# Optimization experiments

Measured on AMD Instinct MI355X. Metric: run time of the kernel, lower is better.

Reference implementation:

```python
import jax, jax.numpy as jnp
import numpy as np

B, C, K, G = 512, 1000, 8, 8   # batch, num classes, boxes per image, grid size
IMG_SIZE = 256.0
L1, L2, L3 = 1.0, 5.0, 1.0     # loss weights (init_kwargs)
LOG_CLAMP = -100.0             # torch BCE clamps log to -100


def setup_inputs() -> dict:
    key = jax.random.key(0)
    k1, k2, k3, k4, k5 = jax.random.split(key, 5)
    # channel 0 is post-sigmoid objectness, so uniform [0,1) is valid for BCE
    outputs = jax.random.uniform(k1, (B, 5 + C, G, G), dtype=jnp.float32)
    boxes = jax.random.uniform(k2, (B, K, 4), dtype=jnp.float32) * IMG_SIZE  # pixel coords
    labels = jax.random.randint(k3, (B, K), 1, C + 1, dtype=jnp.int32)       # 1..C
    box_xy = jax.random.randint(k4, (B, K, 2), 0, G, dtype=jnp.int32)        # (x, y) grid cells
    obj_target = jax.random.uniform(k5, (B, G * G), dtype=jnp.float32)
    return dict(outputs=outputs, boxes=boxes, labels=labels, box_xy=box_xy,
                obj_target=obj_target)


def reference(outputs, boxes, labels, box_xy, obj_target):
    b = outputs.shape[0]

    # ---- objectness BCE (mean over B*64) ----
    p = outputs[:, 0].reshape(b, G * G)
    logp = jnp.maximum(jnp.log(p), LOG_CLAMP)
    log1mp = jnp.maximum(jnp.log1p(-p), LOG_CLAMP)
    cel_obj = -(obj_target * logp + (1.0 - obj_target) * log1mp).mean()

    # ---- gather per-box values at grid cells ----
    bi = jnp.arange(b)[:, None]          # (B,1) broadcasts with (B,K)
    x = box_xy[..., 0]                   # (B,K)
    y = box_xy[..., 1]                   # (B,K)

    # class CE: logits at each box cell, shape (B,K,C)
    cls_logits = outputs[:, 5:][bi, :, y, x]
    ce = jax.nn.logsumexp(cls_logits, axis=-1) - jnp.take_along_axis(
        cls_logits, (labels - 1)[..., None].astype(jnp.int32), axis=-1)[..., 0]
    cel_class = ce.sum() / b             # sum over all boxes, / batch_size

    # bbox MSE: original detaches predictions via .item(), so stop_gradient
    p_box = jax.lax.stop_gradient(outputs[:, 1:5][bi, :, y, x])  # (B,K,4)
    target = jnp.round(boxes / IMG_SIZE * 10.0) / 10.0           # np.round(x/IMG, 1)
    bb_loss = ((p_box - target) ** 2).mean(axis=-1).sum() / b

    total = L1 * cel_obj + L2 * bb_loss + L3 * cel_class
    return total, cel_obj, bb_loss, cel_class
```

## Files before the change

### kernel.cpp

```cpp
#include <hip/hip_runtime.h>
#include <math.h>

#define NB   512
#define NC   1000
#define NK   8
#define PL   64
#define NCH  1005

__global__ __launch_bounds__(512, 4) void yolo_main(
    const float* __restrict__ out,
    const float* __restrict__ boxes,
    const int*   __restrict__ labels,
    const int*   __restrict__ box_xy,
    const float* __restrict__ obj_t,
    float* __restrict__ ws)
{
    const int b    = blockIdx.x;
    const int tid  = threadIdx.x;
    const int w    = tid >> 6;
    const int lane = tid & 63;

    const float*  img = out + (size_t)b * (NCH * PL);
    const float4* p4  = (const float4*)(img + 5 * PL);

    float s0 = 0.f, s1 = 0.f, s2 = 0.f, s3 = 0.f;

    float4 buf[8];
    #pragma unroll
    for (int j = 0; j < 8; ++j) buf[j] = p4[j * 512 + tid];

    #pragma unroll
    for (int t = 0; t < 31; ++t) {
        const float4 v = buf[t & 7];
        if (t < 23) buf[t & 7] = p4[(t + 8) * 512 + tid];
        s0 += __expf(v.x);
        s1 += __expf(v.y);
        s2 += __expf(v.z);
        s3 += __expf(v.w);
    }
    if (tid < 128) {
        const float4 v = p4[15872 + tid];
        s0 += __expf(v.x);
        s1 += __expf(v.y);
        s2 += __expf(v.z);
        s3 += __expf(v.w);
    }

    __shared__ float sm_s[32][64];
    __shared__ float lse_sh[64];
    {
        const int pid = tid >> 4;
        const int q   = tid & 15;
        ((float4*)sm_s[pid])[q] = make_float4(s0, s1, s2, s3);
    }
    __syncthreads();

    float obj_v = 0.f, ce_v = 0.f, bb_v = 0.f;

    if (w == 0) {
        float S = 0.f;
        #pragma unroll
        for (int i = 0; i < 32; ++i) S += sm_s[i][lane];
        lse_sh[lane] = __logf(S);

        const float p   = img[lane];
        const float tt  = obj_t[b * PL + lane];
        const float lp  = fmaxf(__logf(p),  -100.0f);
        const float l1p = fmaxf(log1pf(-p), -100.0f);
        obj_v = -(tt * lp + (1.0f - tt) * l1p);
    }
    __syncthreads();

    if (w == 0 && lane < NK) {
        const int k    = lane;
        const int x    = box_xy[(b * NK + k) * 2 + 0];
        const int y    = box_xy[(b * NK + k) * 2 + 1];
        const int cell = y * 8 + x;
        const int lab  = labels[b * NK + k] - 1;

        const float logit = img[(size_t)(5 + lab) * PL + cell];
        ce_v = lse_sh[cell] - logit;

        float acc = 0.f;
        #pragma unroll
        for (int j = 0; j < 4; ++j) {
            const float pb = img[(size_t)(1 + j) * PL + cell];
            const float tv = rintf(boxes[(b * NK + k) * 4 + j] * (10.0f / 256.0f)) / 10.0f;
            const float d  = pb - tv;
            acc += d * d;
        }
        bb_v = 0.25f * acc;
    }

    if (w == 0) {
        #pragma unroll
        for (int off = 32; off > 0; off >>= 1) {
            obj_v += __shfl_down(obj_v, off);
            ce_v  += __shfl_down(ce_v,  off);
            bb_v  += __shfl_down(bb_v,  off);
        }
        if (lane == 0) {
            ws[b]          = obj_v;
            ws[NB + b]     = ce_v;
            ws[2 * NB + b] = bb_v;
        }
    }
}

__global__ __launch_bounds__(512) void yolo_finish(
    const float* __restrict__ ws, float* __restrict__ dout)
{
    __shared__ float r0[NB], r1[NB], r2[NB];
    const int tid = threadIdx.x;
    r0[tid] = ws[tid];
    r1[tid] = ws[NB + tid];
    r2[tid] = ws[2 * NB + tid];
    __syncthreads();
    for (int off = 256; off > 0; off >>= 1) {
        if (tid < off) {
            r0[tid] += r0[tid + off];
            r1[tid] += r1[tid + off];
            r2[tid] += r2[tid + off];
        }
        __syncthreads();
    }
    if (tid == 0) {
        const float cel_obj   = r0[0] / 32768.0f;
        const float cel_class = r1[0] / 512.0f;
        const float bb_loss   = r2[0] / 512.0f;
        dout[0] = cel_obj + 5.0f * bb_loss + cel_class;
        dout[1] = cel_obj;
        dout[2] = bb_loss;
        dout[3] = cel_class;
    }
}

extern "C" void kernel_launch(void* const* d_in, const int* in_sizes, int n_in,
                              void* d_out, int out_size, void* d_ws, size_t ws_size,
                              hipStream_t stream) {
    const float* outputs = (const float*)d_in[0];
    const float* boxes   = (const float*)d_in[1];
    const int*   labels  = (const int*)d_in[2];
    const int*   box_xy  = (const int*)d_in[3];
    const float* obj_t   = (const float*)d_in[4];
    float* ws   = (float*)d_ws;
    float* dout = (float*)d_out;

    yolo_main<<<NB, 512, 0, stream>>>(outputs, boxes, labels, box_xy, obj_t, ws);
    yolo_finish<<<1, 512, 0, stream>>>(ws, dout);
}
```

Before: 27.67 us.

## Fuse final reduction via last-block atomic counter and hoist gathers before LSE

Merges the separate finish kernel into the main kernel: each block bumps a global counter and the last block to finish reduces the per-block partials and writes the outputs. The scalar gathers (objectness BCE, box MSE, label logit) are also moved ahead of the streaming exp-sum so their latency overlaps with it, which removes one __syncthreads. This trades a second kernel launch for a memset launch plus an atomic and fence per block.

```diff
diff --git a/kernel.cpp b/kernel.cpp
--- a/kernel.cpp
+++ b/kernel.cpp
@@ -7,13 +7,15 @@
 #define PL   64
 #define NCH  1005
 
-__global__ __launch_bounds__(512, 4) void yolo_main(
+__global__ __launch_bounds__(512, 4) void yolo_fused(
     const float* __restrict__ out,
     const float* __restrict__ boxes,
     const int*   __restrict__ labels,
     const int*   __restrict__ box_xy,
     const float* __restrict__ obj_t,
-    float* __restrict__ ws)
+    float* __restrict__ ws,
+    int*   __restrict__ counter,
+    float* __restrict__ dout)
 {
     const int b    = blockIdx.x;
     const int tid  = threadIdx.x;
@@ -23,8 +25,36 @@
     const float*  img = out + (size_t)b * (NCH * PL);
     const float4* p4  = (const float4*)(img + 5 * PL);
 
+    float obj_v = 0.f, ce_v = 0.f, bb_v = 0.f, logit = 0.f;
+    int cell = 0;
+    if (w == 0) {
+        const float p   = img[lane];
+        const float tt  = obj_t[b * PL + lane];
+        const float lp  = fmaxf(__logf(p),  -100.0f);
+        const float l1p = fmaxf(log1pf(-p), -100.0f);
+        obj_v = -(tt * lp + (1.0f - tt) * l1p);
+
+        if (lane < NK) {
+            const int k   = lane;
+            const int x   = box_xy[(b * NK + k) * 2 + 0];
+            const int y   = box_xy[(b * NK + k) * 2 + 1];
+            cell          = y * 8 + x;
+            const int lab = labels[b * NK + k] - 1;
+            logit = img[(size_t)(5 + lab) * PL + cell];
+
+            float acc = 0.f;
+            #pragma unroll
+            for (int j = 0; j < 4; ++j) {
+                const float pb = img[(size_t)(1 + j) * PL + cell];
+                const float tv = rintf(boxes[(b * NK + k) * 4 + j] * (10.0f / 256.0f)) / 10.0f;
+                const float d  = pb - tv;
+                acc += d * d;
+            }
+            bb_v = 0.25f * acc;
+        }
+    }
+
     float s0 = 0.f, s1 = 0.f, s2 = 0.f, s3 = 0.f;
-
     float4 buf[8];
     #pragma unroll
     for (int j = 0; j < 8; ++j) buf[j] = p4[j * 512 + tid];
@@ -55,44 +85,13 @@
     }
     __syncthreads();
 
-    float obj_v = 0.f, ce_v = 0.f, bb_v = 0.f;
-
     if (w == 0) {
         float S = 0.f;
         #pragma unroll
         for (int i = 0; i < 32; ++i) S += sm_s[i][lane];
         lse_sh[lane] = __logf(S);
+        ce_v = (lane < NK) ? (lse_sh[cell] - logit) : 0.f;
 
-        const float p   = img[lane];
-        const float tt  = obj_t[b * PL + lane];
-        const float lp  = fmaxf(__logf(p),  -100.0f);
-        const float l1p = fmaxf(log1pf(-p), -100.0f);
-        obj_v = -(tt * lp + (1.0f - tt) * l1p);
-    }
-    __syncthreads();
-
-    if (w == 0 && lane < NK) {
-        const int k    = lane;
-        const int x    = box_xy[(b * NK + k) * 2 + 0];
-        const int y    = box_xy[(b * NK + k) * 2 + 1];
-        const int cell = y * 8 + x;
-        const int lab  = labels[b * NK + k] - 1;
-
-        const float logit = img[(size_t)(5 + lab) * PL + cell];
-        ce_v = lse_sh[cell] - logit;
-
-        float acc = 0.f;
-        #pragma unroll
-        for (int j = 0; j < 4; ++j) {
-            const float pb = img[(size_t)(1 + j) * PL + cell];
-            const float tv = rintf(boxes[(b * NK + k) * 4 + j] * (10.0f / 256.0f)) / 10.0f;
-            const float d  = pb - tv;
-            acc += d * d;
-        }
-        bb_v = 0.25f * acc;
-    }
-
-    if (w == 0) {
         #pragma unroll
         for (int off = 32; off > 0; off >>= 1) {
             obj_v += __shfl_down(obj_v, off);
@@ -105,33 +104,36 @@
             ws[2 * NB + b] = bb_v;
         }
     }
-}
 
-__global__ __launch_bounds__(512) void yolo_finish(
-    const float* __restrict__ ws, float* __restrict__ dout)
-{
-    __shared__ float r0[NB], r1[NB], r2[NB];
-    const int tid = threadIdx.x;
-    r0[tid] = ws[tid];
-    r1[tid] = ws[NB + tid];
-    r2[tid] = ws[2 * NB + tid];
+    __shared__ int is_last;
+    if (tid == 0) {
+        __threadfence();
+        is_last = (atomicAdd(counter, 1) == NB - 1) ? 1 : 0;
+    }
     __syncthreads();
-    for (int off = 256; off > 0; off >>= 1) {
-        if (tid < off) {
-            r0[tid] += r0[tid + off];
-            r1[tid] += r1[tid + off];
-            r2[tid] += r2[tid + off];
+    if (is_last) {
+        __shared__ float r0[NB], r1[NB], r2[NB];
+        r0[tid] = __hip_atomic_load(&ws[tid],          __ATOMIC_ACQUIRE, __HIP_MEMORY_SCOPE_AGENT);
+        r1[tid] = __hip_atomic_load(&ws[NB + tid],     __ATOMIC_ACQUIRE, __HIP_MEMORY_SCOPE_AGENT);
+        r2[tid] = __hip_atomic_load(&ws[2 * NB + tid], __ATOMIC_ACQUIRE, __HIP_MEMORY_SCOPE_AGENT);
+        __syncthreads();
+        for (int off = 256; off > 0; off >>= 1) {
+            if (tid < off) {
+                r0[tid] += r0[tid + off];
+                r1[tid] += r1[tid + off];
+                r2[tid] += r2[tid + off];
+            }
+            __syncthreads();
         }
-        __syncthreads();
-    }
-    if (tid == 0) {
-        const float cel_obj   = r0[0] / 32768.0f;
-        const float cel_class = r1[0] / 512.0f;
-        const float bb_loss   = r2[0] / 512.0f;
-        dout[0] = cel_obj + 5.0f * bb_loss + cel_class;
-        dout[1] = cel_obj;
-        dout[2] = bb_loss;
-        dout[3] = cel_class;
+        if (tid == 0) {
+            const float cel_obj   = r0[0] / 32768.0f;
+            const float cel_class = r1[0] / 512.0f;
+            const float bb_loss   = r2[0] / 512.0f;
+            dout[0] = cel_obj + 5.0f * bb_loss + cel_class;
+            dout[1] = cel_obj;
+            dout[2] = bb_loss;
+            dout[3] = cel_class;
+        }
     }
 }
 
@@ -143,9 +145,13 @@
     const int*   labels  = (const int*)d_in[2];
     const int*   box_xy  = (const int*)d_in[3];
     const float* obj_t   = (const float*)d_in[4];
-    float* ws   = (float*)d_ws;
-    float* dout = (float*)d_out;
 
-    yolo_main<<<NB, 512, 0, stream>>>(outputs, boxes, labels, box_xy, obj_t, ws);
-    yolo_finish<<<1, 512, 0, stream>>>(ws, dout);
+    float* ws      = (float*)d_ws;
+    int*   counter = (int*)((char*)d_ws + 3 * NB * sizeof(float));
+    float* dout    = (float*)d_out;
+
+    hipMemsetAsync(counter, 0, sizeof(int), stream);
+
+    yolo_fused<<<NB, 512, 0, stream>>>(outputs, boxes, labels, box_xy, obj_t,
+                                       ws, counter, dout);
 }
```

Result: slower. 45.90 us (+65.9%).
